# Optimization experiments

Hardware: AMD Instinct MI355X
Metric: run time of the kernel (lower is better)

## Reference

```python
import jax, jax.numpy as jnp
import numpy as np

DEPTH = 100000


def setup_inputs() -> dict:
    key = jax.random.key(0)
    k1, _ = jax.random.split(key)
    B, S = 1024, 200
    tokens = jax.random.randint(k1, (B, S), 0, DEPTH, dtype=jnp.int32)
    # tf.one_hot on_value=1.0 broadcast to every token position
    on_values = jnp.ones((B, S), dtype=jnp.float32)
    return {"tokens": tokens, "on_values": on_values}


def reference(tokens, on_values):
    """Equivalent to sum(one_hot(tokens, depth), axis=1) -> (B, depth) counts,
    computed via scatter-add without materializing the (B, S, depth) one-hot."""
    B, S = tokens.shape
    tokens = tokens.astype(jnp.int32)
    batch_idx = jnp.arange(B, dtype=jnp.int32)[:, None]  # (B, 1) broadcast over S
    counts = jnp.zeros((B, DEPTH), dtype=jnp.float32)
    counts = counts.at[batch_idx, tokens].add(on_values)
    return counts
```

## Files before the change

kernel.cpp:

```cpp
#include <hip/hip_runtime.h>


#define EMB_DEPTH 100000
#define EMB_SEQ   200
#define NSEG      8
#define SEGSZ     (EMB_DEPTH / NSEG)

__global__ __launch_bounds__(256) void embedder_seg_kernel(
    const int*   __restrict__ tokens,
    const float* __restrict__ on_values,
    float*       __restrict__ out)
{
    __shared__ float cnt[SEGSZ];

    const int tid = threadIdx.x;
    const int b   = blockIdx.x >> 3;
    const int seg = blockIdx.x & (NSEG - 1);
    const int lo  = seg * SEGSZ;

    for (int i = tid; i < SEGSZ; i += 256) cnt[i] = 0.0f;
    __syncthreads();

    if (tid < EMB_SEQ) {
        const int t = tokens[(size_t)b * EMB_SEQ + tid];
        const unsigned r = (unsigned)(t - lo);
        if (r < (unsigned)SEGSZ) {
            atomicAdd(&cnt[r], on_values[(size_t)b * EMB_SEQ + tid]);
        }
    }
    __syncthreads();

    float4* out4 = reinterpret_cast<float4*>(out + (size_t)b * EMB_DEPTH + lo);
    const float4* c4 = reinterpret_cast<const float4*>(cnt);
    #pragma unroll 4
    for (int i = tid; i < SEGSZ / 4; i += 256) {
        out4[i] = c4[i];
    }
}

extern "C" void kernel_launch(void* const* d_in, const int* in_sizes, int n_in,
                              void* d_out, int out_size, void* d_ws, size_t ws_size,
                              hipStream_t stream) {
    const int*   tokens    = (const int*)  d_in[0];
    const float* on_values = (const float*)d_in[1];
    float*       out       = (float*)      d_out;

    const int B = in_sizes[0] / EMB_SEQ;
    embedder_seg_kernel<<<B * NSEG, 256, 0, stream>>>(tokens, on_values, out);
}
```

Baseline: 78.09 us.

## Accumulate per-segment counts in registers instead of a shared-memory histogram

```diff
diff --git a/kernel.cpp b/kernel.cpp
--- a/kernel.cpp
+++ b/kernel.cpp
@@ -4,37 +4,69 @@
 #define EMB_DEPTH 100000
 #define EMB_SEQ   200
 #define NSEG      8
-#define SEGSZ     (EMB_DEPTH / NSEG)
+#define SEGF      (EMB_DEPTH / NSEG)
+#define SEGF4     (SEGF / 4)
+#define NITER     13
 
-__global__ __launch_bounds__(256) void embedder_seg_kernel(
+__global__ __launch_bounds__(256) void embedder_regacc_kernel(
     const int*   __restrict__ tokens,
     const float* __restrict__ on_values,
     float*       __restrict__ out)
 {
-    __shared__ float cnt[SEGSZ];
+    __shared__ int2 sm[EMB_SEQ];
+    __shared__ int  scount;
 
     const int tid = threadIdx.x;
     const int b   = blockIdx.x >> 3;
-    const int seg = blockIdx.x & (NSEG - 1);
-    const int lo  = seg * SEGSZ;
+    const int seg = blockIdx.x & (NSEG-1);
+    const int lo  = seg * SEGF;
 
-    for (int i = tid; i < SEGSZ; i += 256) cnt[i] = 0.0f;
+    if (tid == 0) scount = 0;
     __syncthreads();
 
     if (tid < EMB_SEQ) {
-        const int t = tokens[(size_t)b * EMB_SEQ + tid];
-        const unsigned r = (unsigned)(t - lo);
-        if (r < (unsigned)SEGSZ) {
-            atomicAdd(&cnt[r], on_values[(size_t)b * EMB_SEQ + tid]);
+        const int   t = tokens[(size_t)b * EMB_SEQ + tid];
+        const float v = on_values[(size_t)b * EMB_SEQ + tid];
+        const unsigned rel = (unsigned)(t - lo);
+        if (rel < (unsigned)SEGF) {
+            const int pos = atomicAdd(&scount, 1);
+            sm[pos] = make_int2((int)rel, __float_as_int(v));
         }
     }
+
+    float4 r[NITER];
+    #pragma unroll
+    for (int i = 0; i < NITER; ++i) r[i] = make_float4(0.f, 0.f, 0.f, 0.f);
+
     __syncthreads();
+    const int cnt = scount;
+
+    #pragma unroll 4
+    for (int k = 0; k < cnt; ++k) {
+        const int2 p   = sm[k];
+        const int  rel = p.x;
+        const int  f4  = rel >> 2;
+        if ((f4 & 255) == tid) {
+            const float v = __int_as_float(p.y);
+            const int   j = rel >> 10;
+            const int   c = rel & 3;
+            #pragma unroll
+            for (int i = 0; i < NITER; ++i) {
+                if (j == i) {
+                    r[i].x += (c == 0) ? v : 0.f;
+                    r[i].y += (c == 1) ? v : 0.f;
+                    r[i].z += (c == 2) ? v : 0.f;
+                    r[i].w += (c == 3) ? v : 0.f;
+                }
+            }
+        }
+    }
 
     float4* out4 = reinterpret_cast<float4*>(out + (size_t)b * EMB_DEPTH + lo);
-    const float4* c4 = reinterpret_cast<const float4*>(cnt);
-    #pragma unroll 4
-    for (int i = tid; i < SEGSZ / 4; i += 256) {
-        out4[i] = c4[i];
+    #pragma unroll
+    for (int i = 0; i < NITER; ++i) {
+        const int f4 = i * 256 + tid;
+        if (f4 < SEGF4) out4[f4] = r[i];
     }
 }
 
@@ -46,5 +78,5 @@
     float*       out       = (float*)      d_out;
 
     const int B = in_sizes[0] / EMB_SEQ;
-    embedder_seg_kernel<<<B * NSEG, 256, 0, stream>>>(tokens, on_values, out);
+    embedder_regacc_kernel<<<B * NSEG, 256, 0, stream>>>(tokens, on_values, out);
 }
```

Result: slower. 94.54 us (+21.1%).
